# Kernel optimization log

Hardware: AMD Instinct MI355X
Metric: run time of the kernel (lower is better)

The kernel has to match this reference:

```python
import jax, jax.numpy as jnp
import numpy as np

B, N, K, F, E = 2, 16384, 32, 64, 16


def setup_inputs() -> dict:
    key = jax.random.key(0)
    k1, k2, k3, k4 = jax.random.split(key, 4)
    nodes = jax.random.normal(k1, (B, N, F), dtype=jnp.float32)
    # neighbor list: for each (batch, node) a list of K neighbor node indices
    nlist = jax.random.randint(k2, (B, N, K), 0, N, dtype=jnp.int32)
    edges = jax.random.normal(k3, (B, N, K, E), dtype=jnp.float32)
    # learned weight: (node_feat, node_feat, edge_feat) as in build()
    w = jax.random.normal(k4, (F, F, E), dtype=jnp.float32) * 0.05
    return {"nodes": nodes, "nlist": nlist, "edges": edges, "w": w}


def reference(nodes, nlist, edges, w):
    # tf.gather_nd(nodes, nlist): gather neighbor features -> [B, N, K, F]
    batch_idx = jnp.arange(nodes.shape[0], dtype=nlist.dtype)[:, None, None]
    sliced = nodes[batch_idx, nlist]  # [B, N, K, F]
    # edge-conditioned contraction: edges[b,i,j,n] * sliced[b,i,j,l] * w[l,m,n]
    prod = jnp.einsum('bijn,bijl,lmn->bijm', edges, sliced, w)  # [B, N, K, F]
    # mean over the K neighbors (axis=2); activation is None
    reduced = jnp.mean(prod, axis=2)  # [B, N, F]
    return reduced
```

## Files before the change

kernel.cpp:

```cpp
#include <hip/hip_runtime.h>
#include <cstdint>
#include <cstddef>

#define LOGN 14

typedef __bf16 bf16x8 __attribute__((ext_vector_type(8)));
typedef float f32x4 __attribute__((ext_vector_type(4)));
typedef int   i32x4 __attribute__((ext_vector_type(4)));
typedef unsigned u32;

#define BARRIER() __builtin_amdgcn_s_barrier()
#define LGKM0()   __builtin_amdgcn_s_waitcnt(0xC07F)
#define SFENCE()  __builtin_amdgcn_sched_barrier(0)

__device__ __forceinline__ u32 fbits(float f) { return __builtin_bit_cast(u32, f); }
__device__ __forceinline__ u32 pkrne(float lo, float hi) {
  u32 a = fbits(lo); a = a + 0x7fffu + ((a >> 16) & 1u);
  u32 b = fbits(hi); b = b + 0x7fffu + ((b >> 16) & 1u);
  return (b & 0xffff0000u) | (a >> 16);
}


__global__ void prep_wt(const float* __restrict__ w, unsigned short* __restrict__ wt) {
  int idx = blockIdx.x * 256 + threadIdx.x;
  int m = idx >> 10, k = idx & 1023;
  int ch = k >> 3, wv = k & 7, t = ch >> 4, cc = ch & 15;
  int l = (cc << 2) + (t >> 1), n = ((t & 1) << 3) + wv;
  u32 u = fbits(w[l * 1024 + m * 16 + n] * 0.03125f);
  wt[idx] = (unsigned short)((u + 0x7fffu + ((u >> 16) & 1u)) >> 16);
}

__global__ void prep_nb(const float* __restrict__ nodes, unsigned short* __restrict__ nb) {
  int idx = blockIdx.x * 256 + threadIdx.x;
  const float4* p = (const float4*)nodes + ((size_t)idx << 1);
  float4 a = p[0], b = p[1];
  uint4 o{pkrne(a.x, a.y), pkrne(a.z, a.w), pkrne(b.x, b.y), pkrne(b.z, b.w)};
  *((uint4*)nb + idx) = o;
}

__device__ __forceinline__ bf16x8 mk_bw(const float* wp) {
  float v[8];
  #pragma unroll
  for (int i = 0; i < 8; ++i) v[i] = wp[i] * 0.03125f;
  uint4 pk{pkrne(v[0], v[1]), pkrne(v[2], v[3]), pkrne(v[4], v[5]), pkrne(v[6], v[7])};
  return __builtin_bit_cast(bf16x8, pk);
}

__global__ __launch_bounds__(256, 1)
void mp_fused(const int* __restrict__ nlist, const float* __restrict__ edges,
              const unsigned short* __restrict__ wt, const unsigned short* __restrict__ nb,
              float* __restrict__ out) {
  __shared__ u32 g_lds[2 * 16 * 512];

  const int tid = threadIdx.x;
  const int lane = tid & 63;
  const int wid = __builtin_amdgcn_readfirstlane(tid >> 6);
  const int q = lane >> 4, c = lane & 15;

  const int blk = blockIdx.x;
  const int xcd = blk & 7;
  const int batch = xcd >> 2;
  const int ordinal = ((blk >> 3) << 2) + (xcd & 3);
  const int wg0 = (batch << LOGN) + (ordinal << 6);
  const unsigned short* __restrict__ nbb = nb + ((size_t)batch << 20);

  const int nd0 = wid << 2;
  const int m = (wid << 4) + c;

  bf16x8 wtreg[32];
  {
    const unsigned short* wb = wt + ((size_t)m << 10) + (q << 3);
    #pragma unroll
    for (int s = 0; s < 32; ++s) wtreg[s] = *(const bf16x8*)(wb + (s << 5));
  }

  i32x4 NI[4][2];
  uint2 U[4][8];
  float E[4][8];

  auto issue_nl = [&](int g) {
    #pragma unroll
    for (int j = 0; j < 4; ++j) {
      const int* r = nlist + (((size_t)(g + nd0 + j)) << 5) + (q << 3);
      NI[j][0] = __builtin_nontemporal_load((const i32x4*)r);
      NI[j][1] = __builtin_nontemporal_load((const i32x4*)(r + 4));
    }
  };
  auto issue_se2 = [&](int g, int j0) {
    #pragma unroll
    for (int jj = 0; jj < 2; ++jj) {
      const int j = j0 + jj;
      const int ix[8] = {NI[j][0][0], NI[j][0][1], NI[j][0][2], NI[j][0][3],
                         NI[j][1][0], NI[j][1][1], NI[j][1][2], NI[j][1][3]};
      #pragma unroll
      for (int i = 0; i < 8; ++i)
        U[j][i] = *(const uint2*)(nbb + ((size_t)(u32)ix[i] << 6) + (c << 2));
      const float* ep = edges + (((size_t)(g + nd0 + j)) << 9) + (q << 7) + c;
      #pragma unroll
      for (int i = 0; i < 8; ++i)
        E[j][i] = __builtin_nontemporal_load(ep + (i << 4));
    }
  };
  auto consume_all = [&](int bsel) {
    #pragma unroll
    for (int j = 0; j < 4; ++j) {
      const int p = nd0 + j;
      uint4 apk{pkrne(E[j][0], E[j][1]), pkrne(E[j][2], E[j][3]),
                pkrne(E[j][4], E[j][5]), pkrne(E[j][6], E[j][7])};
      const bf16x8 af = __builtin_bit_cast(bf16x8, apk);
      #pragma unroll
      for (int lt = 0; lt < 4; ++lt) {
        const u32 sel = (lt & 1) ? 0x07060302u : 0x05040100u;
        u32 p0, p1, p2, p3;
        if (lt & 2) {
          p0 = __builtin_amdgcn_perm(U[j][1].y, U[j][0].y, sel);
          p1 = __builtin_amdgcn_perm(U[j][3].y, U[j][2].y, sel);
          p2 = __builtin_amdgcn_perm(U[j][5].y, U[j][4].y, sel);
          p3 = __builtin_amdgcn_perm(U[j][7].y, U[j][6].y, sel);
        } else {
          p0 = __builtin_amdgcn_perm(U[j][1].x, U[j][0].x, sel);
          p1 = __builtin_amdgcn_perm(U[j][3].x, U[j][2].x, sel);
          p2 = __builtin_amdgcn_perm(U[j][5].x, U[j][4].x, sel);
          p3 = __builtin_amdgcn_perm(U[j][7].x, U[j][6].x, sel);
        }
        uint4 spk{p0, p1, p2, p3};
        f32x4 acc{0.f, 0.f, 0.f, 0.f};
        acc = __builtin_amdgcn_mfma_f32_16x16x32_bf16(af,
                __builtin_bit_cast(bf16x8, spk), acc, 0, 0, 0);
        const u32 lo = pkrne(acc[0], acc[1]);
        const u32 hi = pkrne(acc[2], acc[3]);
        const int chunk = (c + (((lt << 1) + (q >> 1)) << 4)) ^ (p & 7);
        *(uint2*)&g_lds[(bsel << 13) + (p << 9) + (chunk << 2) + ((q & 1) << 1)] =
            uint2{lo, hi};
      }
    }
  };
  auto store_out = [&](int g, const f32x4& ob) {
    #pragma unroll
    for (int r = 0; r < 4; ++r)
      __builtin_nontemporal_store(ob[r],
          out + ((size_t)(g + (q << 2) + r) << 6) + m);
  };

  issue_nl(wg0);
  issue_se2(wg0, 0);
  issue_se2(wg0, 2);
  issue_nl(wg0 + 16);
  consume_all(0);
  LGKM0(); BARRIER();

  #pragma unroll
  for (int t = 0; t < 3; ++t) {
    const int gn = wg0 + ((t + 1) << 4);
    issue_se2(gn, 0);
    SFENCE();
    f32x4 ob{0.f, 0.f, 0.f, 0.f};
    #pragma unroll
    for (int s = 0; s < 16; ++s) {
      uint4 ar = *(const uint4*)&g_lds[((t & 1) << 13) + (c << 9) +
                                       ((((s << 2) + q) ^ (c & 7)) << 2)];
      ob = __builtin_amdgcn_mfma_f32_16x16x32_bf16(__builtin_bit_cast(bf16x8, ar),
                                                   wtreg[s], ob, 0, 0, 0);
    }
    issue_se2(gn, 2);
    if (t < 2) issue_nl(wg0 + ((t + 2) << 4));
    SFENCE();
    #pragma unroll
    for (int s = 16; s < 32; ++s) {
      uint4 ar = *(const uint4*)&g_lds[((t & 1) << 13) + (c << 9) +
                                       ((((s << 2) + q) ^ (c & 7)) << 2)];
      ob = __builtin_amdgcn_mfma_f32_16x16x32_bf16(__builtin_bit_cast(bf16x8, ar),
                                                   wtreg[s], ob, 0, 0, 0);
    }
    store_out(wg0 + (t << 4), ob);
    consume_all((t & 1) ^ 1);
    LGKM0(); BARRIER();
  }

  {
    f32x4 ob{0.f, 0.f, 0.f, 0.f};
    #pragma unroll
    for (int s = 0; s < 32; ++s) {
      uint4 ar = *(const uint4*)&g_lds[(1 << 13) + (c << 9) +
                                       ((((s << 2) + q) ^ (c & 7)) << 2)];
      ob = __builtin_amdgcn_mfma_f32_16x16x32_bf16(__builtin_bit_cast(bf16x8, ar),
                                                   wtreg[s], ob, 0, 0, 0);
    }
    store_out(wg0 + 48, ob);
  }
}

template <int MODE>
__global__ __launch_bounds__(256, 3)
void mp_kernel(const float* __restrict__ nodes, const int* __restrict__ nlist,
               const float* __restrict__ edges, const unsigned short* __restrict__ wt,
               const float* __restrict__ w, float* __restrict__ out) {
  __shared__ u32 g_lds[16 * 512];

  const int tid = threadIdx.x;
  const int lane = tid & 63;
  const int wid = __builtin_amdgcn_readfirstlane(tid >> 6);
  const int q = lane >> 4, c = lane & 15;

  const int blk = blockIdx.x;
  const int xcd = blk & 7;
  const int batch = xcd >> 2;
  const int ordinal = ((blk >> 3) << 2) + (xcd & 3);
  const int wg0 = (batch << LOGN) + (ordinal << 4);
  const float* __restrict__ nbase = nodes + ((size_t)batch << 20);

  const int nd0 = wid << 2;

  auto issue_nl = [&](int t, int4* ni) {
    const int* r = nlist + (((size_t)(wg0 + nd0 + t)) << 5) + (q << 3);
    ni[0] = *(const int4*)r;
    ni[1] = *(const int4*)(r + 4);
  };
  auto issue_se = [&](int t, const int4* ni, f32x4* R, float* Ee) {
    const int ix[8] = {ni[0].x, ni[0].y, ni[0].z, ni[0].w,
                       ni[1].x, ni[1].y, ni[1].z, ni[1].w};
    #pragma unroll
    for (int i = 0; i < 8; ++i)
      R[i] = *(const f32x4*)(nbase + ((size_t)(u32)ix[i] << 6) + (c << 2));
    const float* ep = edges + (((size_t)(wg0 + nd0 + t)) << 9) + (q << 7) + c;
    #pragma unroll
    for (int i = 0; i < 8; ++i) Ee[i] = ep[i << 4];
  };
  auto consume = [&](int p, const f32x4* R, const float* Ee) {
    uint4 apk{pkrne(Ee[0], Ee[1]), pkrne(Ee[2], Ee[3]),
              pkrne(Ee[4], Ee[5]), pkrne(Ee[6], Ee[7])};
    const bf16x8 af = __builtin_bit_cast(bf16x8, apk);
    #pragma unroll
    for (int lt = 0; lt < 4; ++lt) {
      uint4 spk{pkrne(R[0][lt], R[1][lt]), pkrne(R[2][lt], R[3][lt]),
                pkrne(R[4][lt], R[5][lt]), pkrne(R[6][lt], R[7][lt])};
      f32x4 acc{0.f, 0.f, 0.f, 0.f};
      acc = __builtin_amdgcn_mfma_f32_16x16x32_bf16(af,
              __builtin_bit_cast(bf16x8, spk), acc, 0, 0, 0);
      const u32 lo = pkrne(acc[0], acc[1]);
      const u32 hi = pkrne(acc[2], acc[3]);
      const int chunk = (c + (((lt << 1) + (q >> 1)) << 4)) ^ (p & 7);
      *(uint2*)&g_lds[(p << 9) + (chunk << 2) + ((q & 1) << 1)] = uint2{lo, hi};
    }
  };

  {
    int4 ni0[2], ni1[2];
    f32x4 R0[8], R1[8];
    float E0[8], E1[8];
    issue_nl(0, ni0);
    issue_nl(1, ni1);
    issue_se(0, ni0, R0, E0);
    issue_nl(2, ni0);
    issue_se(1, ni1, R1, E1);
    issue_nl(3, ni1);
    SFENCE();
    consume(nd0 + 0, R0, E0);
    issue_se(2, ni0, R0, E0);
    SFENCE();
    consume(nd0 + 1, R1, E1);
    issue_se(3, ni1, R1, E1);
    SFENCE();
    consume(nd0 + 2, R0, E0);
    consume(nd0 + 3, R1, E1);
  }

  LGKM0();
  BARRIER();

  const int m = (wid << 4) + c;
  f32x4 ob{0.f, 0.f, 0.f, 0.f};
  if constexpr (MODE >= 1) {
    const unsigned short* wb = wt + ((size_t)m << 10) + (q << 3);
    #pragma unroll 8
    for (int s = 0; s < 32; ++s) {
      uint4 ar = *(const uint4*)&g_lds[(c << 9) + ((((s << 2) + q) ^ (c & 7)) << 2)];
      ob = __builtin_amdgcn_mfma_f32_16x16x32_bf16(__builtin_bit_cast(bf16x8, ar),
                                                   *(const bf16x8*)(wb + (s << 5)),
                                                   ob, 0, 0, 0);
    }
  } else {
    #pragma unroll 4
    for (int s = 0; s < 32; ++s) {
      uint4 ar = *(const uint4*)&g_lds[(c << 9) + ((((s << 2) + q) ^ (c & 7)) << 2)];
      const int ch = (s << 2) + q;
      const int l = ((ch & 15) << 2) + (ch >> 5);
      const int n0 = ((ch >> 4) & 1) << 3;
      const float* wp = w + l * 1024 + m * 16 + n0;
      ob = __builtin_amdgcn_mfma_f32_16x16x32_bf16(__builtin_bit_cast(bf16x8, ar),
                                                   mk_bw(wp), ob, 0, 0, 0);
    }
  }

  #pragma unroll
  for (int r = 0; r < 4; ++r)
    out[((size_t)(wg0 + (q << 2) + r) << 6) + m] = ob[r];
}

extern "C" void kernel_launch(void* const* d_in, const int* in_sizes, int n_in,
                              void* d_out, int out_size, void* d_ws, size_t ws_size,
                              hipStream_t stream) {
  const float* nodes = (const float*)d_in[0];
  const int*   nlist = (const int*)d_in[1];
  const float* edges = (const float*)d_in[2];
  const float* w     = (const float*)d_in[3];
  float* out = (float*)d_out;

  const size_t WT_BYTES = 131072;
  const size_t NB_BYTES = (size_t)1 << 22;

  if (ws_size >= WT_BYTES + NB_BYTES) {
    unsigned short* wt = (unsigned short*)d_ws;
    unsigned short* nb = wt + 65536;
    prep_wt<<<256, 256, 0, stream>>>(w, wt);
    prep_nb<<<1024, 256, 0, stream>>>(nodes, nb);
    mp_fused<<<512, 256, 0, stream>>>(nlist, edges, wt, nb, out);
  } else if (ws_size >= WT_BYTES) {
    unsigned short* wt = (unsigned short*)d_ws;
    prep_wt<<<256, 256, 0, stream>>>(w, wt);
    mp_kernel<1><<<2048, 256, 0, stream>>>(nodes, nlist, edges, wt, w, out);
  } else {
    mp_kernel<0><<<2048, 256, 0, stream>>>(nodes, nlist, edges, nullptr, w, out);
  }
}
```

Baseline: 143.1 us.

## Halve per-block work and LDS in fused kernel to run more blocks per CU

The fused kernel now handles 32 nodes per block instead of 64, launches 1024 blocks, uses a single 32KB LDS buffer instead of a double buffer, and raises launch bounds to 3 blocks per CU. The aim is higher occupancy so latency hiding comes from multiple resident blocks rather than in-block pipelining across four groups. In exchange, each block reloads the 32 weight registers for half the work, adds an extra barrier to reuse the single LDS buffer, and the tighter register budget for 3 blocks/CU may cause spills given the large register arrays.

```diff
diff --git a/kernel.cpp b/kernel.cpp
--- a/kernel.cpp
+++ b/kernel.cpp
@@ -46,11 +46,11 @@
   return __builtin_bit_cast(bf16x8, pk);
 }
 
-__global__ __launch_bounds__(256, 1)
+__global__ __launch_bounds__(256, 3)
 void mp_fused(const int* __restrict__ nlist, const float* __restrict__ edges,
               const unsigned short* __restrict__ wt, const unsigned short* __restrict__ nb,
               float* __restrict__ out) {
-  __shared__ u32 g_lds[2 * 16 * 512];
+  __shared__ u32 g_lds[16 * 512];
 
   const int tid = threadIdx.x;
   const int lane = tid & 63;
@@ -61,7 +61,7 @@
   const int xcd = blk & 7;
   const int batch = xcd >> 2;
   const int ordinal = ((blk >> 3) << 2) + (xcd & 3);
-  const int wg0 = (batch << LOGN) + (ordinal << 6);
+  const int wg0 = (batch << LOGN) + (ordinal << 5);
   const unsigned short* __restrict__ nbb = nb + ((size_t)batch << 20);
 
   const int nd0 = wid << 2;
@@ -101,7 +101,7 @@
         E[j][i] = __builtin_nontemporal_load(ep + (i << 4));
     }
   };
-  auto consume_all = [&](int bsel) {
+  auto consume_all = [&]() {
     #pragma unroll
     for (int j = 0; j < 4; ++j) {
       const int p = nd0 + j;
@@ -130,8 +130,7 @@
         const u32 lo = pkrne(acc[0], acc[1]);
         const u32 hi = pkrne(acc[2], acc[3]);
         const int chunk = (c + (((lt << 1) + (q >> 1)) << 4)) ^ (p & 7);
-        *(uint2*)&g_lds[(bsel << 13) + (p << 9) + (chunk << 2) + ((q & 1) << 1)] =
-            uint2{lo, hi};
+        *(uint2*)&g_lds[(p << 9) + (chunk << 2) + ((q & 1) << 1)] = uint2{lo, hi};
       }
     }
   };
@@ -142,51 +141,47 @@
           out + ((size_t)(g + (q << 2) + r) << 6) + m);
   };
 
-  issue_nl(wg0);
-  issue_se2(wg0, 0);
-  issue_se2(wg0, 2);
-  issue_nl(wg0 + 16);
-  consume_all(0);
+  const int g0 = wg0, g1 = wg0 + 16;
+
+  issue_nl(g0);
+  issue_se2(g0, 0);
+  issue_se2(g0, 2);
+  issue_nl(g1);
+  consume_all();
   LGKM0(); BARRIER();
 
+  issue_se2(g1, 0);
+  SFENCE();
+  f32x4 ob{0.f, 0.f, 0.f, 0.f};
   #pragma unroll
-  for (int t = 0; t < 3; ++t) {
-    const int gn = wg0 + ((t + 1) << 4);
-    issue_se2(gn, 0);
-    SFENCE();
-    f32x4 ob{0.f, 0.f, 0.f, 0.f};
-    #pragma unroll
-    for (int s = 0; s < 16; ++s) {
-      uint4 ar = *(const uint4*)&g_lds[((t & 1) << 13) + (c << 9) +
-                                       ((((s << 2) + q) ^ (c & 7)) << 2)];
-      ob = __builtin_amdgcn_mfma_f32_16x16x32_bf16(__builtin_bit_cast(bf16x8, ar),
-                                                   wtreg[s], ob, 0, 0, 0);
-    }
-    issue_se2(gn, 2);
-    if (t < 2) issue_nl(wg0 + ((t + 2) << 4));
-    SFENCE();
-    #pragma unroll
-    for (int s = 16; s < 32; ++s) {
-      uint4 ar = *(const uint4*)&g_lds[((t & 1) << 13) + (c << 9) +
-                                       ((((s << 2) + q) ^ (c & 7)) << 2)];
-      ob = __builtin_amdgcn_mfma_f32_16x16x32_bf16(__builtin_bit_cast(bf16x8, ar),
-                                                   wtreg[s], ob, 0, 0, 0);
-    }
-    store_out(wg0 + (t << 4), ob);
-    consume_all((t & 1) ^ 1);
-    LGKM0(); BARRIER();
-  }
+  for (int s = 0; s < 16; ++s) {
+    uint4 ar = *(const uint4*)&g_lds[(c << 9) + ((((s << 2) + q) ^ (c & 7)) << 2)];
+    ob = __builtin_amdgcn_mfma_f32_16x16x32_bf16(__builtin_bit_cast(bf16x8, ar),
+                                                 wtreg[s], ob, 0, 0, 0);
+  }
+  issue_se2(g1, 2);
+  SFENCE();
+  #pragma unroll
+  for (int s = 16; s < 32; ++s) {
+    uint4 ar = *(const uint4*)&g_lds[(c << 9) + ((((s << 2) + q) ^ (c & 7)) << 2)];
+    ob = __builtin_amdgcn_mfma_f32_16x16x32_bf16(__builtin_bit_cast(bf16x8, ar),
+                                                 wtreg[s], ob, 0, 0, 0);
+  }
+  store_out(g0, ob);
+
+  BARRIER();
+  consume_all();
+  LGKM0(); BARRIER();
 
   {
-    f32x4 ob{0.f, 0.f, 0.f, 0.f};
+    f32x4 o2{0.f, 0.f, 0.f, 0.f};
     #pragma unroll
     for (int s = 0; s < 32; ++s) {
-      uint4 ar = *(const uint4*)&g_lds[(1 << 13) + (c << 9) +
-                                       ((((s << 2) + q) ^ (c & 7)) << 2)];
-      ob = __builtin_amdgcn_mfma_f32_16x16x32_bf16(__builtin_bit_cast(bf16x8, ar),
-                                                   wtreg[s], ob, 0, 0, 0);
-    }
-    store_out(wg0 + 48, ob);
+      uint4 ar = *(const uint4*)&g_lds[(c << 9) + ((((s << 2) + q) ^ (c & 7)) << 2)];
+      o2 = __builtin_amdgcn_mfma_f32_16x16x32_bf16(__builtin_bit_cast(bf16x8, ar),
+                                                   wtreg[s], o2, 0, 0, 0);
+    }
+    store_out(g1, o2);
   }
 }
 
@@ -314,7 +309,7 @@
     unsigned short* nb = wt + 65536;
     prep_wt<<<256, 256, 0, stream>>>(w, wt);
     prep_nb<<<1024, 256, 0, stream>>>(nodes, nb);
-    mp_fused<<<512, 256, 0, stream>>>(nlist, edges, wt, nb, out);
+    mp_fused<<<1024, 256, 0, stream>>>(nlist, edges, wt, nb, out);
   } else if (ws_size >= WT_BYTES) {
     unsigned short* wt = (unsigned short*)d_ws;
     prep_wt<<<256, 256, 0, stream>>>(w, wt);
```

Result: slower. 218.6 us (+52.8%).
